# Performance work log

Hardware: AMD Instinct MI355X
Metric: run time of the kernel (lower is better)

Reference implementation:

```python
import jax, jax.numpy as jnp
import numpy as np
import math

MAXL = 5
TAUS = [16, 16, 16, 16, 16, 16]
BATCH = 256


def _fact(n):
    return math.factorial(n)


def _cg(l1, l2, l, m1, m2):
    # Standard Clebsch-Gordan coefficient <l1 m1; l2 m2 | l (m1+m2)> (Condon-Shortley)
    m = m1 + m2
    if abs(m) > l or l < abs(l1 - l2) or l > l1 + l2:
        return 0.0
    pref = (2 * l + 1) * _fact(l + l1 - l2) * _fact(l - l1 + l2) * _fact(l1 + l2 - l) / _fact(l1 + l2 + l + 1)
    pref *= _fact(l + m) * _fact(l - m) * _fact(l1 - m1) * _fact(l1 + m1) * _fact(l2 - m2) * _fact(l2 + m2)
    kmin = max(0, -(l - l2 + m1), -(l - l1 - m2))
    kmax = min(l1 + l2 - l, l1 - m1, l2 + m2)
    s = 0.0
    for k in range(kmin, kmax + 1):
        s += ((-1) ** k) / (_fact(k) * _fact(l1 + l2 - l - k) * _fact(l1 - m1 - k)
                            * _fact(l2 + m2 - k) * _fact(l - l2 + m1 + k) * _fact(l - l1 - m2 + k))
    return math.sqrt(pref) * s


def _cg_table(l1, l2, l):
    C = np.zeros((2 * l1 + 1, 2 * l2 + 1, 2 * l + 1), dtype=np.float32)
    for m1 in range(-l1, l1 + 1):
        for m2 in range(-l2, l2 + 1):
            m = m1 + m2
            if abs(m) <= l:
                C[m1 + l1, m2 + l2, m + l] = _cg(l1, l2, l, m1, m2)
    return jnp.asarray(C)


# triples in the exact CUDA-kernel loop order (defines fragment ordering per output l)
_TRIPLES = [(l1, l2, l)
            for l1 in range(MAXL + 1)
            for l2 in range(l1 + 1)
            for l in range(l1 - l2, min(l1 + l2, MAXL) + 1)]
_CG_TABLES = {t: _cg_table(*t) for t in _TRIPLES}


def setup_inputs() -> dict:
    key = jax.random.key(0)
    inp = {}
    for l in range(MAXL + 1):
        key, k = jax.random.split(key)
        inp[f"act{l}"] = jax.random.normal(k, (BATCH, TAUS[l], 2 * l + 1, 2), dtype=jnp.float32)
    return inp


def _cg_forward(acts):
    B = acts[0].shape[0]
    outs = [[] for _ in range(MAXL + 1)]
    for (l1, l2, l) in _TRIPLES:
        C = _CG_TABLES[(l1, l2, l)]  # (2l1+1, 2l2+1, 2l+1)
        A1, A2 = acts[l1], acts[l2]  # (B, tau, 2l*+1, 2) complex as real pairs
        x1, y1 = A1[..., 0], A1[..., 1]
        x2, y2 = A2[..., 0], A2[..., 1]
        # complex outer product of channels, contracted against CG coefficients
        rr = jnp.einsum('bip,bjq,pqm->bijm', x1, x2, C)
        ii = jnp.einsum('bip,bjq,pqm->bijm', y1, y2, C)
        ri = jnp.einsum('bip,bjq,pqm->bijm', x1, y2, C)
        ir = jnp.einsum('bip,bjq,pqm->bijm', y1, x2, C)
        frag = jnp.stack([rr - ii, ri + ir], axis=-1)  # (B, tau1, tau2, 2l+1, 2)
        outs[l].append(frag.reshape(B, -1, 2 * l + 1, 2))
    # per output l: concatenate fragments along channel dim in loop order
    return tuple(jnp.concatenate(fr, axis=1) for fr in outs)


def reference(act0, act1, act2, act3, act4, act5):
    return _cg_forward([act0, act1, act2, act3, act4, act5])
```

## Files before the change

kernel.cpp:

```cpp
#include <hip/hip_runtime.h>


__device__ __constant__ double FACT[17] = {
    1.0, 1.0, 2.0, 6.0, 24.0, 120.0, 720.0, 5040.0, 40320.0, 362880.0,
    3628800.0, 39916800.0, 479001600.0, 6227020800.0, 87178291200.0,
    1307674368000.0, 20922789888000.0};

__device__ double cg_coef(int l1, int l2, int l, int m1, int m2) {
    int m = m1 + m2;
    if (m > l || -m > l || l < l1 - l2 || l > l1 + l2) return 0.0;
    double pref = (double)(2 * l + 1) * FACT[l + l1 - l2] * FACT[l - l1 + l2] *
                  FACT[l1 + l2 - l] / FACT[l1 + l2 + l + 1];
    pref *= FACT[l + m] * FACT[l - m] * FACT[l1 - m1] * FACT[l1 + m1] *
            FACT[l2 - m2] * FACT[l2 + m2];
    int kmin = 0;
    if (-(l - l2 + m1) > kmin) kmin = -(l - l2 + m1);
    if (-(l - l1 - m2) > kmin) kmin = -(l - l1 - m2);
    int kmax = l1 + l2 - l;
    if (l1 - m1 < kmax) kmax = l1 - m1;
    if (l2 + m2 < kmax) kmax = l2 + m2;
    double s = 0.0;
    for (int k = kmin; k <= kmax; ++k) {
        double d = FACT[k] * FACT[l1 + l2 - l - k] * FACT[l1 - m1 - k] *
                   FACT[l2 + m2 - k] * FACT[l - l2 + m1 + k] * FACT[l - l1 - m2 + k];
        s += ((k & 1) ? -1.0 : 1.0) / d;
    }
    return sqrt(pref) * s;
}

constexpr int OUT_BASE[6]  = {0, 786432, 4718592, 13238272, 26083328, 42598400};
constexpr int STRIDE_B[6]  = {3072, 15360, 33280, 50176, 64512, 67584};

constexpr int PL1[21] = {5,5,4,4,5,3,4,3,5,2,4,5,3,2,1,5,4,3,2,1,0};
constexpr int PL2[21] = {5,4,4,3,3,3,2,2,2,2,1,1,1,1,1,0,0,0,0,0,0};
constexpr int PFRAG[21][6] = {
    { 5,  9, 12, 13, 13, 11},
    {-1,  8, 11, 12, 12, 10},
    { 4,  7,  9,  9,  8,  5},
    {-1,  6,  8,  8,  7,  4},
    {-1, -1, 10, 11, 11,  9},
    { 3,  5,  6,  5,  3,  1},
    {-1, -1,  7,  7,  6,  3},
    {-1,  4,  5,  4,  2,  0},
    {-1, -1, -1, 10, 10,  8},
    { 2,  3,  3,  1,  0, -1},
    {-1, -1, -1,  6,  5,  2},
    {-1, -1, -1, -1,  9,  7},
    {-1, -1,  4,  3,  1, -1},
    {-1,  2,  2,  0, -1, -1},
    { 1,  1,  0, -1, -1, -1},
    {-1, -1, -1, -1, -1,  6},
    {-1, -1, -1, -1,  4, -1},
    {-1, -1, -1,  2, -1, -1},
    {-1, -1,  1, -1, -1, -1},
    {-1,  0, -1, -1, -1, -1},
    { 0, -1, -1, -1, -1, -1},
};

template <int PAIR>
__device__ __forceinline__ void pair_body(const float* const acts[6],
                                          float* __restrict__ out,
                                          int b, int tid, float* cg, float* stage) {
    constexpr int L1   = PL1[PAIR];
    constexpr int L2   = PL2[PAIR];
    constexpr int LMIN = L1 - L2;
    constexpr int LMAX = (L1 + L2 < 5) ? (L1 + L2) : 5;
    constexpr int N1   = 2 * L1 + 1;
    constexpr int N2   = 2 * L2 + 1;
    constexpr int NENT = (LMAX - LMIN + 1) * N1 * N2;

    for (int e = tid; e < NENT; e += 256) {
        int li = e / (N1 * N2);
        int r  = e - li * (N1 * N2);
        int p  = r / N2;
        int q  = r - p * N2;
        cg[e] = (float)cg_coef(L1, L2, LMIN + li, p - L1, q - L2);
    }
    __syncthreads();

    int i = tid >> 4;
    int j = tid & 15;

    const float2* __restrict__ z1p =
        (const float2*)(acts[L1] + (size_t)(b * 16 + i) * N1 * 2);
    const float2* __restrict__ z2p =
        (const float2*)(acts[L2] + (size_t)(b * 16 + j) * N2 * 2);
    float2 z1[N1], z2[N2];
#pragma unroll
    for (int p = 0; p < N1; ++p) z1[p] = z1p[p];
#pragma unroll
    for (int q = 0; q < N2; ++q) z2[q] = z2p[q];

#pragma unroll
    for (int l = LMIN; l <= LMAX; ++l) {
        const int NM = 2 * l + 1;
        float ar[11], ai[11];
#pragma unroll
        for (int k = 0; k < NM; ++k) { ar[k] = 0.f; ai[k] = 0.f; }

#pragma unroll
        for (int p = 0; p < N1; ++p) {
#pragma unroll
            for (int q = 0; q < N2; ++q) {
                int m  = (p - L1) + (q - L2);
                int am = m < 0 ? -m : m;
                if (am <= l) {
                    float c  = cg[(l - LMIN) * N1 * N2 + p * N2 + q];
                    float wr = z1[p].x * z2[q].x - z1[p].y * z2[q].y;
                    float wi = z1[p].x * z2[q].y + z1[p].y * z2[q].x;
                    ar[m + l] += c * wr;
                    ai[m + l] += c * wi;
                }
            }
        }

        float2* st = (float2*)stage + tid * NM;
#pragma unroll
        for (int k = 0; k < NM; ++k) st[k] = make_float2(ar[k], ai[k]);
        __syncthreads();

        const float4* __restrict__ s4 = (const float4*)stage;
        float4* __restrict__ d4 = (float4*)(out + OUT_BASE[l] +
            (size_t)b * STRIDE_B[l] + (size_t)PFRAG[PAIR][l] * 512 * NM);
        const int cnt = 128 * NM;
        for (int k = tid; k < cnt; k += 256) d4[k] = s4[k];
        __syncthreads();
    }
}

__global__ __launch_bounds__(256, 4) void fCG_kernel(
    const float* __restrict__ a0, const float* __restrict__ a1,
    const float* __restrict__ a2, const float* __restrict__ a3,
    const float* __restrict__ a4, const float* __restrict__ a5,
    float* __restrict__ out) {
    __shared__ float cg[726];
    __shared__ __align__(16) float stage[5632];
    const float* acts[6] = {a0, a1, a2, a3, a4, a5};
    int pair = blockIdx.x >> 8;
    int b    = blockIdx.x & 255;
    int tid  = threadIdx.x;
    switch (pair) {
        case 0:  pair_body<0>(acts, out, b, tid, cg, stage); break;
        case 1:  pair_body<1>(acts, out, b, tid, cg, stage); break;
        case 2:  pair_body<2>(acts, out, b, tid, cg, stage); break;
        case 3:  pair_body<3>(acts, out, b, tid, cg, stage); break;
        case 4:  pair_body<4>(acts, out, b, tid, cg, stage); break;
        case 5:  pair_body<5>(acts, out, b, tid, cg, stage); break;
        case 6:  pair_body<6>(acts, out, b, tid, cg, stage); break;
        case 7:  pair_body<7>(acts, out, b, tid, cg, stage); break;
        case 8:  pair_body<8>(acts, out, b, tid, cg, stage); break;
        case 9:  pair_body<9>(acts, out, b, tid, cg, stage); break;
        case 10: pair_body<10>(acts, out, b, tid, cg, stage); break;
        case 11: pair_body<11>(acts, out, b, tid, cg, stage); break;
        case 12: pair_body<12>(acts, out, b, tid, cg, stage); break;
        case 13: pair_body<13>(acts, out, b, tid, cg, stage); break;
        case 14: pair_body<14>(acts, out, b, tid, cg, stage); break;
        case 15: pair_body<15>(acts, out, b, tid, cg, stage); break;
        case 16: pair_body<16>(acts, out, b, tid, cg, stage); break;
        case 17: pair_body<17>(acts, out, b, tid, cg, stage); break;
        case 18: pair_body<18>(acts, out, b, tid, cg, stage); break;
        case 19: pair_body<19>(acts, out, b, tid, cg, stage); break;
        case 20: pair_body<20>(acts, out, b, tid, cg, stage); break;
        default: break;
    }
}

extern "C" void kernel_launch(void* const* d_in, const int* in_sizes, int n_in,
                              void* d_out, int out_size, void* d_ws, size_t ws_size,
                              hipStream_t stream) {
    const float* a0 = (const float*)d_in[0];
    const float* a1 = (const float*)d_in[1];
    const float* a2 = (const float*)d_in[2];
    const float* a3 = (const float*)d_in[3];
    const float* a4 = (const float*)d_in[4];
    const float* a5 = (const float*)d_in[5];
    float* out = (float*)d_out;
    fCG_kernel<<<dim3(21 * 256), dim3(256), 0, stream>>>(a0, a1, a2, a3, a4, a5, out);
}
```

Baseline: 321.8 us.

## Bake CG coefficients as compile-time constants and compute each product once for all l

Clebsch-Gordan coefficients are now evaluated at compile time with constexpr recursion, so the per-block double-precision coefficient computation and shared-memory table are gone and zero coefficients are dropped. Each complex product z1[p]*z2[q] is computed once and scattered into the accumulators for every output l, instead of being recomputed per l. Output staging uses two alternating shared buffers so one barrier per l is removed, and l=0 writes go straight to global memory. The trade-off is higher register pressure from holding all accumulators at once, which is why the launch-bounds occupancy hint drops from 4 to 3.

```diff
diff --git a/kernel.cpp b/kernel.cpp
--- a/kernel.cpp
+++ b/kernel.cpp
@@ -1,18 +1,24 @@
 #include <hip/hip_runtime.h>
 
 
-__device__ __constant__ double FACT[17] = {
+constexpr double CFACT[17] = {
     1.0, 1.0, 2.0, 6.0, 24.0, 120.0, 720.0, 5040.0, 40320.0, 362880.0,
     3628800.0, 39916800.0, 479001600.0, 6227020800.0, 87178291200.0,
     1307674368000.0, 20922789888000.0};
 
-__device__ double cg_coef(int l1, int l2, int l, int m1, int m2) {
+constexpr double csqrt_ce(double x) {
+    double g = x > 1.0 ? x : 1.0;
+    for (int i = 0; i < 60; ++i) g = 0.5 * (g + x / g);
+    return g;
+}
+
+constexpr double cg_ce(int l1, int l2, int l, int m1, int m2) {
     int m = m1 + m2;
     if (m > l || -m > l || l < l1 - l2 || l > l1 + l2) return 0.0;
-    double pref = (double)(2 * l + 1) * FACT[l + l1 - l2] * FACT[l - l1 + l2] *
-                  FACT[l1 + l2 - l] / FACT[l1 + l2 + l + 1];
-    pref *= FACT[l + m] * FACT[l - m] * FACT[l1 - m1] * FACT[l1 + m1] *
-            FACT[l2 - m2] * FACT[l2 + m2];
+    double pref = (double)(2 * l + 1) * CFACT[l + l1 - l2] * CFACT[l - l1 + l2] *
+                  CFACT[l1 + l2 - l] / CFACT[l1 + l2 + l + 1];
+    pref *= CFACT[l + m] * CFACT[l - m] * CFACT[l1 - m1] * CFACT[l1 + m1] *
+            CFACT[l2 - m2] * CFACT[l2 + m2];
     int kmin = 0;
     if (-(l - l2 + m1) > kmin) kmin = -(l - l2 + m1);
     if (-(l - l1 - m2) > kmin) kmin = -(l - l1 - m2);
@@ -21,11 +27,11 @@
     if (l2 + m2 < kmax) kmax = l2 + m2;
     double s = 0.0;
     for (int k = kmin; k <= kmax; ++k) {
-        double d = FACT[k] * FACT[l1 + l2 - l - k] * FACT[l1 - m1 - k] *
-                   FACT[l2 + m2 - k] * FACT[l - l2 + m1 + k] * FACT[l - l1 - m2 + k];
+        double d = CFACT[k] * CFACT[l1 + l2 - l - k] * CFACT[l1 - m1 - k] *
+                   CFACT[l2 + m2 - k] * CFACT[l - l2 + m1 + k] * CFACT[l - l1 - m2 + k];
         s += ((k & 1) ? -1.0 : 1.0) / d;
     }
-    return sqrt(pref) * s;
+    return csqrt_ce(pref) * s;
 }
 
 constexpr int OUT_BASE[6]  = {0, 786432, 4718592, 13238272, 26083328, 42598400};
@@ -57,29 +63,54 @@
     { 0, -1, -1, -1, -1, -1},
 };
 
+
+template <int L1, int L2, int P, int Q, int LV>
+__device__ __forceinline__ void accum_l(float wr, float wi, float* ar, float* ai) {
+    constexpr int LMIN = L1 - L2;
+    constexpr int LMAX = (L1 + L2 < 5) ? (L1 + L2) : 5;
+    constexpr int M  = (P - L1) + (Q - L2);
+    constexpr int AM = M < 0 ? -M : M;
+    if constexpr (AM <= LV) {
+        constexpr float c = (float)cg_ce(L1, L2, LV, P - L1, Q - L2);
+        if constexpr (c != 0.0f) {
+            constexpr int idx = LV * LV - LMIN * LMIN + M + LV;
+            ar[idx] += c * wr;
+            ai[idx] += c * wi;
+        }
+    }
+    if constexpr (LV < LMAX) accum_l<L1, L2, P, Q, LV + 1>(wr, wi, ar, ai);
+}
+
+template <int L1, int L2, int P, int Q>
+__device__ __forceinline__ void do_q(const float2* z1, const float2* z2,
+                                     float* ar, float* ai) {
+    float wr = z1[P].x * z2[Q].x - z1[P].y * z2[Q].y;
+    float wi = z1[P].x * z2[Q].y + z1[P].y * z2[Q].x;
+    accum_l<L1, L2, P, Q, L1 - L2>(wr, wi, ar, ai);
+    if constexpr (Q + 1 < 2 * L2 + 1) do_q<L1, L2, P, Q + 1>(z1, z2, ar, ai);
+}
+
+template <int L1, int L2, int P>
+__device__ __forceinline__ void do_p(const float2* z1, const float2* z2,
+                                     float* ar, float* ai) {
+    do_q<L1, L2, P, 0>(z1, z2, ar, ai);
+    if constexpr (P + 1 < 2 * L1 + 1) do_p<L1, L2, P + 1>(z1, z2, ar, ai);
+}
+
 template <int PAIR>
 __device__ __forceinline__ void pair_body(const float* const acts[6],
                                           float* __restrict__ out,
-                                          int b, int tid, float* cg, float* stage) {
+                                          int b, int tid, float* stage) {
     constexpr int L1   = PL1[PAIR];
     constexpr int L2   = PL2[PAIR];
     constexpr int LMIN = L1 - L2;
     constexpr int LMAX = (L1 + L2 < 5) ? (L1 + L2) : 5;
     constexpr int N1   = 2 * L1 + 1;
     constexpr int N2   = 2 * L2 + 1;
-    constexpr int NENT = (LMAX - LMIN + 1) * N1 * N2;
-
-    for (int e = tid; e < NENT; e += 256) {
-        int li = e / (N1 * N2);
-        int r  = e - li * (N1 * N2);
-        int p  = r / N2;
-        int q  = r - p * N2;
-        cg[e] = (float)cg_coef(L1, L2, LMIN + li, p - L1, q - L2);
-    }
-    __syncthreads();
-
-    int i = tid >> 4;
-    int j = tid & 15;
+    constexpr int NTOT = (LMAX + 1) * (LMAX + 1) - LMIN * LMIN;
+
+    const int i = tid >> 4;
+    const int j = tid & 15;
 
     const float2* __restrict__ z1p =
         (const float2*)(acts[L1] + (size_t)(b * 16 + i) * N1 * 2);
@@ -91,76 +122,68 @@
 #pragma unroll
     for (int q = 0; q < N2; ++q) z2[q] = z2p[q];
 
+    float ar[NTOT], ai[NTOT];
+#pragma unroll
+    for (int k = 0; k < NTOT; ++k) { ar[k] = 0.f; ai[k] = 0.f; }
+
+    do_p<L1, L2, 0>(z1, z2, ar, ai);
+
 #pragma unroll
     for (int l = LMIN; l <= LMAX; ++l) {
-        const int NM = 2 * l + 1;
-        float ar[11], ai[11];
-#pragma unroll
-        for (int k = 0; k < NM; ++k) { ar[k] = 0.f; ai[k] = 0.f; }
-
-#pragma unroll
-        for (int p = 0; p < N1; ++p) {
-#pragma unroll
-            for (int q = 0; q < N2; ++q) {
-                int m  = (p - L1) + (q - L2);
-                int am = m < 0 ? -m : m;
-                if (am <= l) {
-                    float c  = cg[(l - LMIN) * N1 * N2 + p * N2 + q];
-                    float wr = z1[p].x * z2[q].x - z1[p].y * z2[q].y;
-                    float wi = z1[p].x * z2[q].y + z1[p].y * z2[q].x;
-                    ar[m + l] += c * wr;
-                    ai[m + l] += c * wi;
-                }
-            }
+        const int NM   = 2 * l + 1;
+        const int off  = l * l - LMIN * LMIN;
+        const int frag = PFRAG[PAIR][l];
+        if (NM == 1) {
+            float2* __restrict__ d2 = (float2*)(out + OUT_BASE[l] +
+                (size_t)b * STRIDE_B[l] + (size_t)frag * 512);
+            d2[tid] = make_float2(ar[off], ai[off]);
+        } else {
+            float* sb = stage + (size_t)((l - LMIN) & 1) * 5632;
+            float2* st = (float2*)sb + tid * NM;
+#pragma unroll
+            for (int k = 0; k < NM; ++k) st[k] = make_float2(ar[off + k], ai[off + k]);
+            __syncthreads();
+            const float4* __restrict__ s4 = (const float4*)sb;
+            float4* __restrict__ d4 = (float4*)(out + OUT_BASE[l] +
+                (size_t)b * STRIDE_B[l] + (size_t)frag * 512 * NM);
+            const int cnt = 128 * NM;
+            for (int k = tid; k < cnt; k += 256) d4[k] = s4[k];
         }
-
-        float2* st = (float2*)stage + tid * NM;
-#pragma unroll
-        for (int k = 0; k < NM; ++k) st[k] = make_float2(ar[k], ai[k]);
-        __syncthreads();
-
-        const float4* __restrict__ s4 = (const float4*)stage;
-        float4* __restrict__ d4 = (float4*)(out + OUT_BASE[l] +
-            (size_t)b * STRIDE_B[l] + (size_t)PFRAG[PAIR][l] * 512 * NM);
-        const int cnt = 128 * NM;
-        for (int k = tid; k < cnt; k += 256) d4[k] = s4[k];
-        __syncthreads();
-    }
-}
-
-__global__ __launch_bounds__(256, 4) void fCG_kernel(
+    }
+}
+
+__global__ __launch_bounds__(256, 3) void fCG_kernel(
     const float* __restrict__ a0, const float* __restrict__ a1,
     const float* __restrict__ a2, const float* __restrict__ a3,
     const float* __restrict__ a4, const float* __restrict__ a5,
     float* __restrict__ out) {
-    __shared__ float cg[726];
-    __shared__ __align__(16) float stage[5632];
+    __shared__ __align__(16) float stage[2 * 5632];
     const float* acts[6] = {a0, a1, a2, a3, a4, a5};
     int pair = blockIdx.x >> 8;
     int b    = blockIdx.x & 255;
     int tid  = threadIdx.x;
     switch (pair) {
-        case 0:  pair_body<0>(acts, out, b, tid, cg, stage); break;
-        case 1:  pair_body<1>(acts, out, b, tid, cg, stage); break;
-        case 2:  pair_body<2>(acts, out, b, tid, cg, stage); break;
-        case 3:  pair_body<3>(acts, out, b, tid, cg, stage); break;
-        case 4:  pair_body<4>(acts, out, b, tid, cg, stage); break;
-        case 5:  pair_body<5>(acts, out, b, tid, cg, stage); break;
-        case 6:  pair_body<6>(acts, out, b, tid, cg, stage); break;
-        case 7:  pair_body<7>(acts, out, b, tid, cg, stage); break;
-        case 8:  pair_body<8>(acts, out, b, tid, cg, stage); break;
-        case 9:  pair_body<9>(acts, out, b, tid, cg, stage); break;
-        case 10: pair_body<10>(acts, out, b, tid, cg, stage); break;
-        case 11: pair_body<11>(acts, out, b, tid, cg, stage); break;
-        case 12: pair_body<12>(acts, out, b, tid, cg, stage); break;
-        case 13: pair_body<13>(acts, out, b, tid, cg, stage); break;
-        case 14: pair_body<14>(acts, out, b, tid, cg, stage); break;
-        case 15: pair_body<15>(acts, out, b, tid, cg, stage); break;
-        case 16: pair_body<16>(acts, out, b, tid, cg, stage); break;
-        case 17: pair_body<17>(acts, out, b, tid, cg, stage); break;
-        case 18: pair_body<18>(acts, out, b, tid, cg, stage); break;
-        case 19: pair_body<19>(acts, out, b, tid, cg, stage); break;
-        case 20: pair_body<20>(acts, out, b, tid, cg, stage); break;
+        case 0:  pair_body<0>(acts, out, b, tid, stage); break;
+        case 1:  pair_body<1>(acts, out, b, tid, stage); break;
+        case 2:  pair_body<2>(acts, out, b, tid, stage); break;
+        case 3:  pair_body<3>(acts, out, b, tid, stage); break;
+        case 4:  pair_body<4>(acts, out, b, tid, stage); break;
+        case 5:  pair_body<5>(acts, out, b, tid, stage); break;
+        case 6:  pair_body<6>(acts, out, b, tid, stage); break;
+        case 7:  pair_body<7>(acts, out, b, tid, stage); break;
+        case 8:  pair_body<8>(acts, out, b, tid, stage); break;
+        case 9:  pair_body<9>(acts, out, b, tid, stage); break;
+        case 10: pair_body<10>(acts, out, b, tid, stage); break;
+        case 11: pair_body<11>(acts, out, b, tid, stage); break;
+        case 12: pair_body<12>(acts, out, b, tid, stage); break;
+        case 13: pair_body<13>(acts, out, b, tid, stage); break;
+        case 14: pair_body<14>(acts, out, b, tid, stage); break;
+        case 15: pair_body<15>(acts, out, b, tid, stage); break;
+        case 16: pair_body<16>(acts, out, b, tid, stage); break;
+        case 17: pair_body<17>(acts, out, b, tid, stage); break;
+        case 18: pair_body<18>(acts, out, b, tid, stage); break;
+        case 19: pair_body<19>(acts, out, b, tid, stage); break;
+        case 20: pair_body<20>(acts, out, b, tid, stage); break;
         default: break;
     }
 }
```

After: 261.9 us (median of 2 runs). 1.23x faster.
